# Optimization experiments

Hardware: AMD Instinct MI355X
Metric: run time of the kernel (lower is better)

## Reference

```python
import jax, jax.numpy as jnp
import numpy as np

IN_DIM = 784   # 28*28
N_FEAT = 100
MW = 20
MP = 100
S = 30
N = 2048
BETA = 0.9
THRESH = 1.0


def setup_inputs() -> dict:
    key = jax.random.key(0)
    ks = jax.random.split(key, 6)
    X = jax.random.uniform(ks[0], (N, IN_DIM), jnp.float32)
    r1 = (1.0 / IN_DIM) ** 0.5
    W1 = jax.random.uniform(ks[1], (IN_DIM, N_FEAT), jnp.float32, -r1, r1)
    B1 = jax.random.uniform(ks[2], (N_FEAT,), jnp.float32, -r1, r1)
    r2 = (1.0 / N_FEAT) ** 0.5
    # all mw windows concatenated: (n_feat, mw*mp)
    W2 = jax.random.uniform(ks[3], (N_FEAT, MW * MP), jnp.float32, -r2, r2)
    B2 = jax.random.uniform(ks[4], (MW * MP,), jnp.float32, -r2, r2)
    # uniform noise for Bernoulli rate coding (spikegen.rate)
    U = jax.random.uniform(ks[5], (S, N, N_FEAT), jnp.float32)
    return {"X": X, "W1": W1, "B1": B1, "W2": W2, "B2": B2, "U": U}


def reference(X, W1, B1, W2, B2, U):
    # Feature layer: linear -> sigmoid(./3) -> Bernoulli rate-coded spikes
    Z_prob = jax.nn.sigmoid((X @ W1 + B1) / 3.0)          # (N, F)
    Z_spk = (U < Z_prob[None]).astype(X.dtype)             # (S, N, F) in {0,1}

    # Enhancement: one GEMM per run covering all windows (LIF is elementwise,
    # so concatenating the mw window weight matrices is exact).
    H_pre = jnp.einsum('snf,fp->snp', Z_spk, W2) + B2      # (S, N, MW*MP)

    # LIF (snn.Leaky, reset-by-subtraction):
    #   mem_t = beta*mem_{t-1} + x_t - spk_{t-1}*thresh ; spk_t = (mem_t > thresh)
    def step(carry, x):
        mem, spk = carry
        mem = BETA * mem + x - spk * THRESH
        spk = (mem > THRESH).astype(x.dtype)
        return (mem, spk), spk

    z0 = jnp.zeros(H_pre.shape[1:], H_pre.dtype)
    _, H_spk = jax.lax.scan(step, (z0, z0), H_pre)         # (S, N, MW*MP)

    # Rate aggregation over time, then concat [Z | H]
    A = jnp.concatenate([Z_spk.mean(axis=0), H_spk.mean(axis=0)], axis=1)
    return A  # (N, N_FEAT + MW*MP)
```

## Files before the change

### kernel.cpp

```cpp
#include <hip/hip_runtime.h>

#define NN      2048
#define IN_DIM  784
#define NFEAT   100
#define NP      2000
#define NS      30
#define OUTC    2100
#define NWIN    5
#define G4      4
#define GB      4
#define CHUNK   64

typedef double f64x4  __attribute__((ext_vector_type(4)));
typedef float  f32x4  __attribute__((ext_vector_type(4)));
typedef short  bf16x8 __attribute__((ext_vector_type(8)));

#define AS1 __attribute__((address_space(1)))
#define AS3 __attribute__((address_space(3)))

__device__ __forceinline__ void stage16(const void* g, void* l) {
    __builtin_amdgcn_global_load_lds((const AS1 unsigned int*)g,
                                     (AS3 unsigned int*)l, 16, 0, 0);
}

#define VMWAIT0()                                                   \
    {                                                               \
        asm volatile("s_waitcnt vmcnt(0)" ::: "memory");            \
        __builtin_amdgcn_sched_barrier(0);                          \
    }

__device__ __forceinline__ f64x4 mfma_f64(double a, double b, f64x4 c) {
#if __has_builtin(__builtin_amdgcn_mfma_f64_16x16x4f64)
    return __builtin_amdgcn_mfma_f64_16x16x4f64(a, b, c, 0, 0, 0);
#else
    asm volatile("v_mfma_f64_16x16x4_f64 %0, %1, %2, %0"
                 : "+v"(c) : "v"(a), "v"(b));
    return c;
#endif
}

__global__ __launch_bounds__(128) void sbls_k1(
    const float* __restrict__ X, const float* __restrict__ W1,
    const float* __restrict__ B1, const float* __restrict__ U,
    float* __restrict__ out, unsigned* __restrict__ colmask)
{
    __shared__ float xs[IN_DIM];
    const int n = blockIdx.x;
    const int t = threadIdx.x;

    for (int k = t; k < IN_DIM; k += 128)
        xs[k] = X[(size_t)n * IN_DIM + k];
    __syncthreads();

    if (t >= NFEAT) return;
    const int f = t;

    double a0 = 0.0, a1 = 0.0, a2 = 0.0, a3 = 0.0;
    for (int k = 0; k < IN_DIM; k += 4) {
        a0 += (double)xs[k + 0] * (double)W1[(k + 0) * NFEAT + f];
        a1 += (double)xs[k + 1] * (double)W1[(k + 1) * NFEAT + f];
        a2 += (double)xs[k + 2] * (double)W1[(k + 2) * NFEAT + f];
        a3 += (double)xs[k + 3] * (double)W1[(k + 3) * NFEAT + f];
    }
    double acc = (double)B1[f] + ((a0 + a1) + (a2 + a3));
    double z = 1.0 / (1.0 + exp(-acc / 3.0));

    unsigned m = 0;
    int cnt = 0;
    for (int s = 0; s < NS; ++s) {
        float u = U[(size_t)s * (NN * NFEAT) + (size_t)n * NFEAT + f];
        int sp = ((double)u < z) ? 1 : 0;
        m |= (unsigned)sp << s;
        cnt += sp;
    }
    colmask[n * NFEAT + f] = m;
    out[(size_t)n * OUTC + f] = (float)((double)cnt / 30.0);
}

__global__ __launch_bounds__(256) void sbls_slice(
    const float* __restrict__ W2, unsigned short* __restrict__ slt)
{
    int idx = blockIdx.x * blockDim.x + threadIdx.x;
    if (idx >= NP * 128) return;
    int f = idx & 127;
    int p = idx >> 7;

    double w = (f < NFEAT) ? (double)W2[(size_t)f * NP + p] : 0.0;
    double aw = fabs(w);
    double sg = (w < 0.0) ? -1.0 : 1.0;
    double r = aw;
    const double scale[NWIN] = {0x1p11, 0x1p19, 0x1p27, 0x1p35, 0x1p43};
#pragma unroll
    for (int j = 0; j < NWIN; ++j) {
        double t = floor(r * scale[j]);
        r = r - t / scale[j];
        float v = (float)(sg * t / scale[j]);
        unsigned u = __builtin_bit_cast(unsigned, v);
        slt[((size_t)j * NP + p) * 128 + f] = (unsigned short)(u >> 16);
    }
}

__global__ __launch_bounds__(256) void sbls_afrag4(
    const unsigned* __restrict__ colmask, unsigned short* __restrict__ afragG)
{
    __shared__ unsigned smask[G4][NFEAT];
    const int ng = blockIdx.x;
    const int t  = threadIdx.x;

    for (int i = t; i < G4 * NFEAT; i += 256)
        smask[i / NFEAT][i % NFEAT] = colmask[ng * G4 * NFEAT + i];
    __syncthreads();

    for (int e = t; e < 32 * 64; e += 256) {
        int fid = e >> 6, L = e & 63;
        int st = fid & 1, n = (fid >> 1) & 3, kt = fid >> 3;
        int lgE = L >> 4, lmE = L & 15;
        int s = st * 16 + lmE;
        bf16x8 v;
#pragma unroll
        for (int j = 0; j < 8; ++j) {
            int f = kt * 32 + lgE * 8 + j;
            unsigned mv = (f < NFEAT) ? smask[n][f] : 0u;
            v[j] = (short)(((mv >> s) & 1u) ? 0x3F80 : 0);
        }
        *(bf16x8*)(afragG + ((size_t)ng * 32 + fid) * 64 * 8 + (size_t)L * 8) = v;
    }
}

union ShA {
    unsigned short b[2][NWIN][64][32];
    double h[2][32][67];
};

__global__ __launch_bounds__(256, 3) void sbls_k2_ga(
    const unsigned short* __restrict__ slt,
    const unsigned short* __restrict__ afragG,
    const float*    __restrict__ B2,
    float*          __restrict__ out)
{
    __shared__ __align__(16) ShA sh;

    const int lid  = blockIdx.y * 512 + blockIdx.x;
    const int xcd  = lid & 7;
    const int idx  = lid >> 3;
    const int chunk = idx & 31;
    const int ng    = xcd * 64 + (idx >> 5);

    const int t  = threadIdx.x;
    const int l  = t & 63;
    const int wv = t >> 6;
    const int lm = l & 15;
    const int lg = l >> 4;

    const int plw = wv * 16 + (l >> 2);
    const int pw  = chunk * CHUNK + plw;
    const int prw = (pw < NP) ? pw : (NP - 1);
    const int fgw = ((l & 3) - ((l >> 3) & 3)) & 3;
    const unsigned short* sbase = slt + (size_t)prw * 128 + fgw * 8;

    const unsigned short* ag = afragG + (size_t)ng * 32 * 64 * 8;

    const int prd = wv * 16 + lm;
    const int slot0 = (lm >> 1) & 3;

#define STAGE(buf, kt)                                                        \
    {                                                                         \
        _Pragma("unroll")                                                     \
        for (int w = 0; w < NWIN; ++w)                                        \
            stage16(sbase + (size_t)w * NP * 128 + (kt) * 32,                 \
                    &sh.b[buf][w][wv * 16][0]);                               \
    }

    f32x4 acc[3][2][G4];
#pragma unroll
    for (int wp = 0; wp < 3; ++wp)
#pragma unroll
        for (int st = 0; st < 2; ++st)
#pragma unroll
            for (int n = 0; n < G4; ++n)
                acc[wp][st][n] = (f32x4){0.f, 0.f, 0.f, 0.f};

    STAGE(0, 0)
    bf16x8 acur[G4][2];
#pragma unroll
    for (int n = 0; n < G4; ++n)
#pragma unroll
        for (int st = 0; st < 2; ++st)
            acur[n][st] = *(const bf16x8*)(
                ag + ((size_t)((0 * G4 + n) * 2 + st) * 64 + l) * 8);
    VMWAIT0()

#pragma unroll
    for (int kt = 0; kt < 4; ++kt) {
        const int buf = kt & 1;
        if (kt < 3) STAGE(buf ^ 1, kt + 1)

        bf16x8 b[NWIN];
#pragma unroll
        for (int w = 0; w < NWIN; ++w) {
            const int slot = (lg + slot0) & 3;
            b[w] = *(const bf16x8*)(&sh.b[buf][w][prd][slot * 8]);
        }

        __builtin_amdgcn_s_setprio(1);
#pragma unroll
        for (int w = 0; w < NWIN; ++w)
#pragma unroll
            for (int n = 0; n < G4; ++n)
#pragma unroll
                for (int st = 0; st < 2; ++st)
                    acc[w >> 1][st][n] = __builtin_amdgcn_mfma_f32_16x16x32_bf16(
                        acur[n][st], b[w], acc[w >> 1][st][n], 0, 0, 0);
        __builtin_amdgcn_s_setprio(0);

        if (kt < 3) {
#pragma unroll
            for (int n = 0; n < G4; ++n)
#pragma unroll
                for (int st = 0; st < 2; ++st)
                    acur[n][st] = *(const bf16x8*)(
                        ag + ((size_t)(((kt + 1) * G4 + n) * 2 + st) * 64 + l) * 8);
            VMWAIT0()
        }
    }
#undef STAGE

    __syncthreads();
#pragma unroll
    for (int np2 = 0; np2 < 2; ++np2) {
#pragma unroll
        for (int nn = 0; nn < 2; ++nn) {
            const int n = np2 * 2 + nn;
#pragma unroll
            for (int st = 0; st < 2; ++st)
#pragma unroll
                for (int r = 0; r < 4; ++r) {
                    double hv = (double)acc[0][st][n][r]
                              + (double)acc[1][st][n][r]
                              + (double)acc[2][st][n][r];
                    sh.h[nn][st * 16 + lg * 4 + r][wv * 16 + lm] = hv;
                }
        }
        __syncthreads();
        if (t < 128) {
            const int nn = t >> 6;
            const int pl = t & 63;
            const int pp = chunk * CHUNK + pl;
            if (pp < NP) {
                double b2d = (double)B2[pp];
                double mem = 0.0, spk = 0.0;
                int cnt = 0;
#pragma unroll
                for (int s = 0; s < NS; ++s) {
                    double hh = sh.h[nn][s][pl] + b2d;
                    mem = 0.9 * mem + hh - spk;
                    bool sp = mem > 1.0;
                    spk = sp ? 1.0 : 0.0;
                    cnt += sp;
                }
                out[(size_t)(ng * G4 + np2 * 2 + nn) * OUTC + NFEAT + pp] =
                    (float)((double)cnt / 30.0);
            }
        }
        if (np2 == 0) __syncthreads();
    }
}

__global__ __launch_bounds__(256, 2) void sbls_k2_bf16(
    const unsigned short* __restrict__ slt,
    const float*    __restrict__ B2,
    const unsigned* __restrict__ colmask,
    float*          __restrict__ out)
{
    __shared__ unsigned smask[GB][NFEAT];
    union ShU {
        unsigned short afrag[32][64][8];
        double h[GB][32][67];
    };
    __shared__ __align__(16) ShU shu;

    const int ng    = blockIdx.x;
    const int chunk = blockIdx.y;
    const int t  = threadIdx.x;
    const int l  = t & 63;
    const int wv = t >> 6;
    const int lm = l & 15;
    const int lg = l >> 4;

    for (int i = t; i < GB * NFEAT; i += 256)
        smask[i / NFEAT][i % NFEAT] = colmask[(ng * GB + i / NFEAT) * NFEAT + (i % NFEAT)];
    __syncthreads();

    for (int e = t; e < 32 * 64; e += 256) {
        int fid = e >> 6, L = e & 63;
        int st = fid & 1, n = (fid >> 1) & 3, kt = fid >> 3;
        int lgE = L >> 4, lmE = L & 15;
        int s = st * 16 + lmE;
        bf16x8 v;
#pragma unroll
        for (int j = 0; j < 8; ++j) {
            int f = kt * 32 + lgE * 8 + j;
            unsigned mv = (f < NFEAT) ? smask[n][f] : 0u;
            v[j] = (short)(((mv >> s) & 1u) ? 0x3F80 : 0);
        }
        *(bf16x8*)(&shu.afrag[fid][L][0]) = v;
    }
    __syncthreads();

    const int p = chunk * CHUNK + wv * 16 + lm;
    const int prow = (p < NP) ? p : (NP - 1);
    const unsigned short* bbase = slt + (size_t)prow * 128 + lg * 8;

    f32x4 acc[3][2][GB];
#pragma unroll
    for (int wp = 0; wp < 3; ++wp)
#pragma unroll
        for (int st = 0; st < 2; ++st)
#pragma unroll
            for (int n = 0; n < GB; ++n)
                acc[wp][st][n] = (f32x4){0.f, 0.f, 0.f, 0.f};

    bf16x8 bcur[NWIN], bnxt[NWIN];
#pragma unroll
    for (int w = 0; w < NWIN; ++w)
        bcur[w] = *(const bf16x8*)(bbase + (size_t)w * NP * 128);

#pragma unroll
    for (int kt = 0; kt < 4; ++kt) {
        bf16x8 a[GB][2];
#pragma unroll
        for (int n = 0; n < GB; ++n)
#pragma unroll
            for (int st = 0; st < 2; ++st)
                a[n][st] = *(const bf16x8*)(&shu.afrag[(kt * GB + n) * 2 + st][l][0]);

        if (kt < 3) {
#pragma unroll
            for (int w = 0; w < NWIN; ++w)
                bnxt[w] = *(const bf16x8*)(bbase + (size_t)w * NP * 128 + (kt + 1) * 32);
        }

#pragma unroll
        for (int w = 0; w < NWIN; ++w)
#pragma unroll
            for (int n = 0; n < GB; ++n)
#pragma unroll
                for (int st = 0; st < 2; ++st)
                    acc[w >> 1][st][n] = __builtin_amdgcn_mfma_f32_16x16x32_bf16(
                        a[n][st], bcur[w], acc[w >> 1][st][n], 0, 0, 0);

        if (kt < 3) {
#pragma unroll
            for (int w = 0; w < NWIN; ++w) bcur[w] = bnxt[w];
        }
    }

    __syncthreads();
#pragma unroll
    for (int n = 0; n < GB; ++n)
#pragma unroll
        for (int st = 0; st < 2; ++st)
#pragma unroll
            for (int r = 0; r < 4; ++r) {
                double hv = (double)acc[0][st][n][r]
                          + (double)acc[1][st][n][r]
                          + (double)acc[2][st][n][r];
                shu.h[n][st * 16 + lg * 4 + r][wv * 16 + lm] = hv;
            }
    __syncthreads();
    {
        const int nn = t >> 6;
        const int pl = t & 63;
        const int pp = chunk * CHUNK + pl;
        if (pp < NP) {
            double b2d = (double)B2[pp];
            double mem = 0.0, spk = 0.0;
            int cnt = 0;
#pragma unroll
            for (int s = 0; s < NS; ++s) {
                double hh = shu.h[nn][s][pl] + b2d;
                mem = 0.9 * mem + hh - spk;
                bool sp = mem > 1.0;
                spk = sp ? 1.0 : 0.0;
                cnt += sp;
            }
            out[(size_t)(ng * GB + nn) * OUTC + NFEAT + pp] = (float)((double)cnt / 30.0);
        }
    }
}

__global__ __launch_bounds__(256, 2) void sbls_k2_f64(
    const float*    __restrict__ W2, const float* __restrict__ B2,
    const unsigned* __restrict__ colmask, float* __restrict__ out)
{
    __shared__ unsigned smask[NFEAT];
    __shared__ double h_lds[32][130];

    const int n     = blockIdx.x;
    const int chunk = blockIdx.y;
    const int l  = threadIdx.x & 63;
    const int wv = threadIdx.x >> 6;
    const int lm = l & 15;
    const int lg = l >> 4;

    if (threadIdx.x < NFEAT)
        smask[threadIdx.x] = colmask[n * NFEAT + threadIdx.x];

    f64x4 zero = (f64x4){0.0, 0.0, 0.0, 0.0};
    f64x4 d1 = mfma_f64((double)lm, 1.0, zero);
    f64x4 d2 = mfma_f64(1.0, (double)lm, zero);
    int srow[4], pcol[4];
#pragma unroll
    for (int r = 0; r < 4; ++r) {
        int a = (int)(d1[r] * 0.25);
        int b = (int)(d2[r] * 0.25);
        srow[r] = (a < 0) ? 0 : (a > 15 ? 15 : a);
        pcol[r] = (b < 0) ? 0 : (b > 15 ? 15 : b);
    }
    __syncthreads();

    f64x4 acc[2][4];
    int pclamp[4];
#pragma unroll
    for (int i = 0; i < 4; ++i) {
        int p = chunk * 256 + (wv * 4 + i) * 16 + lm;
        pclamp[i] = (p < NP) ? p : (NP - 1);
        acc[0][i] = zero; acc[1][i] = zero;
    }
    for (int kt = 0; kt < 25; ++kt) {
        unsigned mw = smask[kt * 4 + lg];
        double a0 = ((mw >> lm) & 1u) ? 1.0 : 0.0;
        double a1 = ((mw >> (lm + 16)) & 1u) ? 1.0 : 0.0;
        const float* wrow = W2 + (size_t)(kt * 4 + lg) * NP;
#pragma unroll
        for (int i = 0; i < 4; ++i) {
            double b = (double)wrow[pclamp[i]];
            acc[0][i] = mfma_f64(a0, b, acc[0][i]);
            acc[1][i] = mfma_f64(a1, b, acc[1][i]);
        }
    }
#pragma unroll
    for (int hp = 0; hp < 2; ++hp) {
        __syncthreads();
        if ((wv >> 1) == hp) {
#pragma unroll
            for (int i = 0; i < 4; ++i) {
                int tloc = (wv & 1) * 4 + i;
#pragma unroll
                for (int st = 0; st < 2; ++st)
#pragma unroll
                    for (int r = 0; r < 4; ++r)
                        h_lds[st * 16 + srow[r]][tloc * 16 + pcol[r]] = acc[st][i][r];
            }
        }
        __syncthreads();
        if (threadIdx.x < 128) {
            int p = chunk * 256 + hp * 128 + threadIdx.x;
            if (p < NP) {
                double b2d = (double)B2[p];
                double mem = 0.0, spk = 0.0;
                int cnt = 0;
#pragma unroll
                for (int s = 0; s < NS; ++s) {
                    double hh = h_lds[s][threadIdx.x] + b2d;
                    mem = 0.9 * mem + hh - spk;
                    bool sp = mem > 1.0;
                    spk = sp ? 1.0 : 0.0;
                    cnt += sp;
                }
                out[(size_t)n * OUTC + NFEAT + p] = (float)((double)cnt / 30.0);
            }
        }
    }
}

extern "C" void kernel_launch(void* const* d_in, const int* in_sizes, int n_in,
                              void* d_out, int out_size, void* d_ws, size_t ws_size,
                              hipStream_t stream) {
    const float* X  = (const float*)d_in[0];
    const float* W1 = (const float*)d_in[1];
    const float* B1 = (const float*)d_in[2];
    const float* W2 = (const float*)d_in[3];
    const float* B2 = (const float*)d_in[4];
    const float* U  = (const float*)d_in[5];
    float* out = (float*)d_out;

    unsigned* colmask = (unsigned*)d_ws;
    const size_t SLT_OFF   = 1u << 20;
    const size_t SLT_BYTES = (size_t)NWIN * NP * 128 * 2;
    const size_t AF_OFF    = 4u << 20;
    const size_t AF_BYTES  = (size_t)(NN / G4) * 32 * 64 * 8 * 2;
    unsigned short* slt    = (unsigned short*)((char*)d_ws + SLT_OFF);
    unsigned short* afragG = (unsigned short*)((char*)d_ws + AF_OFF);
    bool tierA = (ws_size >= AF_OFF + AF_BYTES);
    bool tierB = (ws_size >= SLT_OFF + SLT_BYTES);

    sbls_k1<<<NN, 128, 0, stream>>>(X, W1, B1, U, out, colmask);

    if (tierA) {
        sbls_slice<<<(NP * 128 + 255) / 256, 256, 0, stream>>>(W2, slt);
        sbls_afrag4<<<NN / G4, 256, 0, stream>>>(colmask, afragG);
        dim3 grid(512, 32);
        sbls_k2_ga<<<grid, 256, 0, stream>>>(slt, afragG, B2, out);
    } else if (tierB) {
        sbls_slice<<<(NP * 128 + 255) / 256, 256, 0, stream>>>(W2, slt);
        dim3 grid(NN / GB, (NP + CHUNK - 1) / CHUNK);
        sbls_k2_bf16<<<grid, 256, 0, stream>>>(slt, B2, colmask, out);
    } else {
        dim3 grid(NN, (NP + 255) / 256);
        sbls_k2_f64<<<grid, 256, 0, stream>>>(W2, B2, colmask, out);
    }
}
```

Measured before the change: 211.2 us.

## Block four rows per feature-layer CTA and relax vmcnt waits in GEMM

The feature-layer kernel now gives each block four input rows instead of one. Each W1 element loaded from global memory is reused for four fp64 accumulators, and the grid shrinks fourfold. Separately, the enhancement GEMM's waits go from vmcnt(0) to vmcnt(8). That waits only for the older LDS staging loads and lets the eight newest A-fragment register loads stay in flight, which is intended to overlap them with work. The trade-offs are less parallelism in the first kernel and reliance on the compiler's own waitcnt before the A fragments are used.

```diff
diff --git a/kernel.cpp b/kernel.cpp
--- a/kernel.cpp
+++ b/kernel.cpp
@@ -10,6 +10,7 @@
 #define G4      4
 #define GB      4
 #define CHUNK   64
+#define K1G     4
 
 typedef double f64x4  __attribute__((ext_vector_type(4)));
 typedef float  f32x4  __attribute__((ext_vector_type(4)));
@@ -23,9 +24,9 @@
                                      (AS3 unsigned int*)l, 16, 0, 0);
 }
 
-#define VMWAIT0()                                                   \
+#define VMWAIT8()                                                   \
     {                                                               \
-        asm volatile("s_waitcnt vmcnt(0)" ::: "memory");            \
+        asm volatile("s_waitcnt vmcnt(8)" ::: "memory");            \
         __builtin_amdgcn_sched_barrier(0);                          \
     }
 
@@ -44,37 +45,46 @@
     const float* __restrict__ B1, const float* __restrict__ U,
     float* __restrict__ out, unsigned* __restrict__ colmask)
 {
-    __shared__ float xs[IN_DIM];
-    const int n = blockIdx.x;
+    __shared__ float xs[K1G][IN_DIM];
+    const int ngrp = blockIdx.x;
     const int t = threadIdx.x;
-
-    for (int k = t; k < IN_DIM; k += 128)
-        xs[k] = X[(size_t)n * IN_DIM + k];
-    __syncthreads();
-
+    const int n0 = ngrp * K1G;
+
+    for (int i = t; i < K1G * IN_DIM; i += 128) {
+        int nn = i / IN_DIM, k = i - nn * IN_DIM;
+        xs[nn][k] = X[(size_t)(n0 + nn) * IN_DIM + k];
+    }
+    __syncthreads();
     if (t >= NFEAT) return;
     const int f = t;
 
-    double a0 = 0.0, a1 = 0.0, a2 = 0.0, a3 = 0.0;
-    for (int k = 0; k < IN_DIM; k += 4) {
-        a0 += (double)xs[k + 0] * (double)W1[(k + 0) * NFEAT + f];
-        a1 += (double)xs[k + 1] * (double)W1[(k + 1) * NFEAT + f];
-        a2 += (double)xs[k + 2] * (double)W1[(k + 2) * NFEAT + f];
-        a3 += (double)xs[k + 3] * (double)W1[(k + 3) * NFEAT + f];
-    }
-    double acc = (double)B1[f] + ((a0 + a1) + (a2 + a3));
-    double z = 1.0 / (1.0 + exp(-acc / 3.0));
-
-    unsigned m = 0;
-    int cnt = 0;
-    for (int s = 0; s < NS; ++s) {
-        float u = U[(size_t)s * (NN * NFEAT) + (size_t)n * NFEAT + f];
-        int sp = ((double)u < z) ? 1 : 0;
-        m |= (unsigned)sp << s;
-        cnt += sp;
-    }
-    colmask[n * NFEAT + f] = m;
-    out[(size_t)n * OUTC + f] = (float)((double)cnt / 30.0);
+    double acc[K1G];
+#pragma unroll
+    for (int nn = 0; nn < K1G; ++nn) acc[nn] = 0.0;
+
+#pragma unroll 4
+    for (int k = 0; k < IN_DIM; ++k) {
+        double w = (double)W1[k * NFEAT + f];
+#pragma unroll
+        for (int nn = 0; nn < K1G; ++nn)
+            acc[nn] += (double)xs[nn][k] * w;
+    }
+
+    const double b = (double)B1[f];
+#pragma unroll
+    for (int nn = 0; nn < K1G; ++nn) {
+        double z = 1.0 / (1.0 + exp(-(acc[nn] + b) / 3.0));
+        unsigned m = 0;
+        int cnt = 0;
+        for (int s = 0; s < NS; ++s) {
+            float u = U[(size_t)s * (NN * NFEAT) + (size_t)(n0 + nn) * NFEAT + f];
+            int sp = ((double)u < z) ? 1 : 0;
+            m |= (unsigned)sp << s;
+            cnt += sp;
+        }
+        colmask[(n0 + nn) * NFEAT + f] = m;
+        out[(size_t)(n0 + nn) * OUTC + f] = (float)((double)cnt / 30.0);
+    }
 }
 
 __global__ __launch_bounds__(256) void sbls_slice(
@@ -188,7 +198,7 @@
         for (int st = 0; st < 2; ++st)
             acur[n][st] = *(const bf16x8*)(
                 ag + ((size_t)((0 * G4 + n) * 2 + st) * 64 + l) * 8);
-    VMWAIT0()
+    VMWAIT8()
 
 #pragma unroll
     for (int kt = 0; kt < 4; ++kt) {
@@ -220,7 +230,7 @@
                 for (int st = 0; st < 2; ++st)
                     acur[n][st] = *(const bf16x8*)(
                         ag + ((size_t)(((kt + 1) * G4 + n) * 2 + st) * 64 + l) * 8);
-            VMWAIT0()
+            VMWAIT8()
         }
     }
 #undef STAGE
@@ -495,7 +505,7 @@
     bool tierA = (ws_size >= AF_OFF + AF_BYTES);
     bool tierB = (ws_size >= SLT_OFF + SLT_BYTES);
 
-    sbls_k1<<<NN, 128, 0, stream>>>(X, W1, B1, U, out, colmask);
+    sbls_k1<<<NN / K1G, 128, 0, stream>>>(X, W1, B1, U, out, colmask);
 
     if (tierA) {
         sbls_slice<<<(NP * 128 + 255) / 256, 256, 0, stream>>>(W2, slt);
```

Result: slower. 231.6 us (+9.7%).
